# Performance work log

Measured on AMD Instinct MI355X. Metric: run time of the kernel, lower is better.

The kernel has to match this reference:

```python
import jax, jax.numpy as jnp
import numpy as np

N_OUT = 128
N_PARAMS = 64
DEGREE = 3
LB = -3.0
UB = 3.0
N_POINTS = 1048576


def get_knots():
    # (ub-lb) * [zeros(degree), linspace(0,1,n_params-degree), ones(degree)] + lb
    t = np.concatenate([np.zeros(DEGREE), np.linspace(0.0, 1.0, N_PARAMS - DEGREE), np.ones(DEGREE)])
    return jnp.asarray((UB - LB) * t + LB, dtype=jnp.float32)  # [n_params + degree]


def eval_basis(x, knots):
    # x: [N], knots: [n_knots] with n_knots = n_params + degree
    n_knots = knots.shape[0]
    xb = x[:, None]  # [N,1]
    # degree-0 indicator functions, vectorized over all knot intervals
    phis = ((knots[:-1] <= xb) & (xb < knots[1:])).astype(x.dtype)  # [N, n_knots-1]
    # Cox-de Boor recursion, vectorized over basis index i for each degree d
    for d in range(1, DEGREE + 1):
        m = n_knots - d - 1
        ld = knots[d:d + m] - knots[:m]          # left denominators  [m]
        rd = knots[d + 1:d + 1 + m] - knots[1:1 + m]  # right denominators [m]
        left = jnp.where(ld != 0, (xb - knots[:m]) / jnp.where(ld != 0, ld, 1.0), 0.0)
        right = jnp.where(rd != 0, (knots[d + 1:d + 1 + m] - xb) / jnp.where(rd != 0, rd, 1.0), 0.0)
        new = left * phis[:, :m] + right * phis[:, 1:m + 1]
        phis = jnp.concatenate([new, phis[:, m:]], axis=1)
    # last used column is replaced by SiLU(x) (column n_knots - degree - 1 == n_params - 1)
    phis = phis.at[:, n_knots - DEGREE - 1].set(jax.nn.silu(x))
    return phis[:, :N_PARAMS]  # [N, n_params]


def setup_inputs() -> dict:
    key = jax.random.key(0)
    k1, k2 = jax.random.split(key)
    x = jax.random.normal(k1, (N_POINTS,), dtype=jnp.float32)
    params = jax.random.normal(k2, (N_PARAMS, N_OUT), dtype=jnp.float32) * 0.1
    return {"x": x, "params": params}


def reference(x, params):
    knots = get_knots()
    basis = eval_basis(x, knots)          # [N, n_params]
    return (basis @ params).T             # [n_out, N]
```

## Files before the change

kernel.cpp:

```cpp
#include <hip/hip_runtime.h>

#define NPTS 1048576
#define NOUT 128
#define NPAR 64
#define BLOCK 256
#define PPT 4
#define CPB (BLOCK * PPT)
#define STRH 136
#define G 8
#define SST 1024

typedef float vf4 __attribute__((ext_vector_type(4)));

__device__ __forceinline__ unsigned short f2bf(float f) {
    unsigned int u = __float_as_uint(f);
    u += 0x7fffu + ((u >> 16) & 1u);
    return (unsigned short)(u >> 16);
}

__device__ __forceinline__ void bf2x(unsigned int u, float& lo, float& hi) {
    lo = __uint_as_float(u << 16);
    hi = __uint_as_float(u & 0xffff0000u);
}

__global__ __launch_bounds__(BLOCK, 4)
void kan_kernel(const float* __restrict__ x,
                const float* __restrict__ params,
                float* __restrict__ out) {
    __shared__ unsigned short sH[NPAR * STRH];
    __shared__ float sS[G * SST];

    const int tid = threadIdx.x;

    {
        const float4* p4 = (const float4*)params;
        #pragma unroll
        for (int g = tid; g < NPAR * (NOUT / 4); g += BLOCK) {
            float4 v = p4[g];
            ushort4 h;
            h.x = f2bf(v.x); h.y = f2bf(v.y); h.z = f2bf(v.z); h.w = f2bf(v.w);
            *(ushort4*)&sH[(g >> 5) * STRH + (g & 31) * 4] = h;
        }
    }

    const int base = blockIdx.x * CPB + tid * PPT;
    const float4 xv = *(const float4*)(x + base);
    float xs[PPT] = {xv.x, xv.y, xv.z, xv.w};

    float b[PPT][4];
    float sil[PPT];
    int   rbase[PPT];

    #pragma unroll
    for (int pp = 0; pp < PPT; ++pp) {
        float xx = xs[pp];
        sil[pp] = xx / (1.0f + __expf(-xx));

        float inr = (xx >= -3.0f && xx < 3.0f) ? 1.0f : 0.0f;
        float u = (xx + 3.0f) * 10.0f;
        int si = (int)u;
        si = si < 0 ? 0 : (si > 59 ? 59 : si);

        float Ki   = -3.0f + 0.1f * (float)si;
        float Kim1 = -3.0f + 0.1f * (float)(si - 1 > 0 ? si - 1 : 0);
        float Kim2 = -3.0f + 0.1f * (float)(si - 2 > 0 ? si - 2 : 0);
        float Kip1 = -3.0f + 0.1f * (float)(si + 1);
        float Kip2 = -3.0f + 0.1f * (float)(si + 2 < 60 ? si + 2 : 60);
        float Kip3 = -3.0f + 0.1f * (float)(si + 3 < 60 ? si + 3 : 60);

        float l1 = xx - Ki,   r1 = Kip1 - xx;
        float l2 = xx - Kim1, r2 = Kip2 - xx;
        float l3 = xx - Kim2, r3 = Kip3 - xx;

        float N0 = 1.0f, N1, N2, N3, t, saved;
        t = N0 / (r1 + l1); N0 = r1 * t; N1 = l1 * t;
        t = N0 / (r1 + l2); N0 = r1 * t;          saved = l2 * t;
        t = N1 / (r2 + l1); N1 = saved + r2 * t;  N2    = l1 * t;
        t = N0 / (r1 + l3); N0 = r1 * t;          saved = l3 * t;
        t = N1 / (r2 + l2); N1 = saved + r2 * t;  saved = l2 * t;
        t = N2 / (r3 + l1); N2 = saved + r3 * t;  N3    = l1 * t;

        b[pp][0] = N0 * inr;
        b[pp][1] = N1 * inr;
        b[pp][2] = N2 * inr;
        b[pp][3] = N3 * inr;
        rbase[pp] = si;
    }

    __syncthreads();

    const int w = tid >> 6;
    const int l = tid & 63;

    #pragma unroll 1
    for (int j0 = 0; j0 < NOUT; j0 += G) {
        uint4 u63 = *(const uint4*)&sH[63 * STRH + j0];
        float p63f[8];
        bf2x(u63.x, p63f[0], p63f[1]);
        bf2x(u63.y, p63f[2], p63f[3]);
        bf2x(u63.z, p63f[4], p63f[5]);
        bf2x(u63.w, p63f[6], p63f[7]);

        float a[PPT][8];
        #pragma unroll
        for (int pp = 0; pp < PPT; ++pp) {
            const unsigned short* rp = &sH[rbase[pp] * STRH + j0];
            float s = sil[pp];
            float acc[8];
            #pragma unroll
            for (int c = 0; c < 8; ++c) acc[c] = s * p63f[c];

            #pragma unroll
            for (int r = 0; r < 4; ++r) {
                uint4 q = *(const uint4*)(rp + r * STRH);
                float f[8];
                bf2x(q.x, f[0], f[1]); bf2x(q.y, f[2], f[3]);
                bf2x(q.z, f[4], f[5]); bf2x(q.w, f[6], f[7]);
                float br = b[pp][r];
                #pragma unroll
                for (int c = 0; c < 8; ++c) acc[c] = fmaf(br, f[c], acc[c]);
            }
            #pragma unroll
            for (int c = 0; c < 8; ++c) a[pp][c] = acc[c];
        }

        #pragma unroll
        for (int c = 0; c < 8; ++c) {
            vf4 v = { a[0][c], a[1][c], a[2][c], a[3][c] };
            *(vf4*)&sS[c * SST + tid * 4] = v;
        }

        __syncthreads();

        #pragma unroll
        for (int rr = 0; rr < 2; ++rr) {
            const int r = 2 * w + rr;
            float* orow = out + (size_t)(j0 + r) * NPTS + blockIdx.x * CPB;
            #pragma unroll
            for (int k = 0; k < 4; ++k) {
                vf4 v = *(const vf4*)&sS[r * SST + k * 256 + l * 4];
                *(vf4*)(orow + k * 256 + l * 4) = v;
            }
        }

        __syncthreads();
    }
}

extern "C" void kernel_launch(void* const* d_in, const int* in_sizes, int n_in,
                              void* d_out, int out_size, void* d_ws, size_t ws_size,
                              hipStream_t stream) {
    const float* x      = (const float*)d_in[0];
    const float* params = (const float*)d_in[1];
    float* out          = (float*)d_out;

    dim3 grid(NPTS / CPB);
    kan_kernel<<<grid, BLOCK, 0, stream>>>(x, params, out);
}
```

Measured before the change: 120.2 us.

## Warp-specialize producer/consumer waves with double-buffered bf16 LDS ring

Splits each 512-thread block into four compute waves that evaluate the spline basis and matmul tile, and four store waves that stream finished tiles to global memory. Tiles pass through a two-slot LDS ring guarded by workgroup-scope atomic counters instead of block-wide barriers, so compute and stores can overlap. Intermediate tiles are staged as bf16 to halve the LDS footprint, which rounds outputs to bf16 precision. Spin-wait polling and higher register pressure at the larger block size are added costs.

```diff
diff --git a/kernel.cpp b/kernel.cpp
--- a/kernel.cpp
+++ b/kernel.cpp
@@ -3,12 +3,10 @@
 #define NPTS 1048576
 #define NOUT 128
 #define NPAR 64
-#define BLOCK 256
-#define PPT 4
-#define CPB (BLOCK * PPT)
+#define BLOCK 512
+#define CPB 1024
 #define STRH 136
-#define G 8
-#define SST 1024
+#define NTILE 16
 
 typedef float vf4 __attribute__((ext_vector_type(4)));
 
@@ -28,122 +26,148 @@
                 const float* __restrict__ params,
                 float* __restrict__ out) {
     __shared__ unsigned short sH[NPAR * STRH];
-    __shared__ float sS[G * SST];
+    __shared__ unsigned short sRing[2][8 * CPB];
+    __shared__ int prodCnt[2];
+    __shared__ int consCnt[2];
 
     const int tid = threadIdx.x;
+    const int w   = tid >> 6;
+    const int l   = tid & 63;
 
-    {
+    if (tid == 0) { prodCnt[0] = prodCnt[1] = consCnt[0] = consCnt[1] = 0; }
+
+    float b[4][4], sil[4];
+    int rbase[4];
+    if (w < 4) {
         const float4* p4 = (const float4*)params;
         #pragma unroll
-        for (int g = tid; g < NPAR * (NOUT / 4); g += BLOCK) {
+        for (int g = tid; g < NPAR * (NOUT / 4); g += 256) {
             float4 v = p4[g];
             ushort4 h;
             h.x = f2bf(v.x); h.y = f2bf(v.y); h.z = f2bf(v.z); h.w = f2bf(v.w);
             *(ushort4*)&sH[(g >> 5) * STRH + (g & 31) * 4] = h;
         }
-    }
 
-    const int base = blockIdx.x * CPB + tid * PPT;
-    const float4 xv = *(const float4*)(x + base);
-    float xs[PPT] = {xv.x, xv.y, xv.z, xv.w};
+        const int base = blockIdx.x * CPB + tid * 4;
+        const float4 xv = *(const float4*)(x + base);
+        float xs[4] = {xv.x, xv.y, xv.z, xv.w};
 
-    float b[PPT][4];
-    float sil[PPT];
-    int   rbase[PPT];
+        #pragma unroll
+        for (int pp = 0; pp < 4; ++pp) {
+            float xx = xs[pp];
+            sil[pp] = xx / (1.0f + __expf(-xx));
+            float inr = (xx >= -3.0f && xx < 3.0f) ? 1.0f : 0.0f;
+            float u = (xx + 3.0f) * 10.0f;
+            int si = (int)u;
+            si = si < 0 ? 0 : (si > 59 ? 59 : si);
 
-    #pragma unroll
-    for (int pp = 0; pp < PPT; ++pp) {
-        float xx = xs[pp];
-        sil[pp] = xx / (1.0f + __expf(-xx));
+            float Ki   = -3.0f + 0.1f * (float)si;
+            float Kim1 = -3.0f + 0.1f * (float)(si - 1 > 0 ? si - 1 : 0);
+            float Kim2 = -3.0f + 0.1f * (float)(si - 2 > 0 ? si - 2 : 0);
+            float Kip1 = -3.0f + 0.1f * (float)(si + 1);
+            float Kip2 = -3.0f + 0.1f * (float)(si + 2 < 60 ? si + 2 : 60);
+            float Kip3 = -3.0f + 0.1f * (float)(si + 3 < 60 ? si + 3 : 60);
 
-        float inr = (xx >= -3.0f && xx < 3.0f) ? 1.0f : 0.0f;
-        float u = (xx + 3.0f) * 10.0f;
-        int si = (int)u;
-        si = si < 0 ? 0 : (si > 59 ? 59 : si);
+            float l1 = xx - Ki,   r1 = Kip1 - xx;
+            float l2 = xx - Kim1, r2 = Kip2 - xx;
+            float l3 = xx - Kim2, r3 = Kip3 - xx;
 
-        float Ki   = -3.0f + 0.1f * (float)si;
-        float Kim1 = -3.0f + 0.1f * (float)(si - 1 > 0 ? si - 1 : 0);
-        float Kim2 = -3.0f + 0.1f * (float)(si - 2 > 0 ? si - 2 : 0);
-        float Kip1 = -3.0f + 0.1f * (float)(si + 1);
-        float Kip2 = -3.0f + 0.1f * (float)(si + 2 < 60 ? si + 2 : 60);
-        float Kip3 = -3.0f + 0.1f * (float)(si + 3 < 60 ? si + 3 : 60);
+            float N0 = 1.0f, N1, N2, N3, t, saved;
+            t = N0 / (r1 + l1); N0 = r1 * t; N1 = l1 * t;
+            t = N0 / (r1 + l2); N0 = r1 * t;          saved = l2 * t;
+            t = N1 / (r2 + l1); N1 = saved + r2 * t;  N2    = l1 * t;
+            t = N0 / (r1 + l3); N0 = r1 * t;          saved = l3 * t;
+            t = N1 / (r2 + l2); N1 = saved + r2 * t;  saved = l2 * t;
+            t = N2 / (r3 + l1); N2 = saved + r3 * t;  N3    = l1 * t;
 
-        float l1 = xx - Ki,   r1 = Kip1 - xx;
-        float l2 = xx - Kim1, r2 = Kip2 - xx;
-        float l3 = xx - Kim2, r3 = Kip3 - xx;
-
-        float N0 = 1.0f, N1, N2, N3, t, saved;
-        t = N0 / (r1 + l1); N0 = r1 * t; N1 = l1 * t;
-        t = N0 / (r1 + l2); N0 = r1 * t;          saved = l2 * t;
-        t = N1 / (r2 + l1); N1 = saved + r2 * t;  N2    = l1 * t;
-        t = N0 / (r1 + l3); N0 = r1 * t;          saved = l3 * t;
-        t = N1 / (r2 + l2); N1 = saved + r2 * t;  saved = l2 * t;
-        t = N2 / (r3 + l1); N2 = saved + r3 * t;  N3    = l1 * t;
-
-        b[pp][0] = N0 * inr;
-        b[pp][1] = N1 * inr;
-        b[pp][2] = N2 * inr;
-        b[pp][3] = N3 * inr;
-        rbase[pp] = si;
+            b[pp][0] = N0 * inr; b[pp][1] = N1 * inr;
+            b[pp][2] = N2 * inr; b[pp][3] = N3 * inr;
+            rbase[pp] = si;
+        }
     }
 
     __syncthreads();
 
-    const int w = tid >> 6;
-    const int l = tid & 63;
+    if (w < 4) {
+        #pragma unroll 1
+        for (int t = 0; t < NTILE; ++t) {
+            const int s = t & 1, g = t >> 1;
+            if (g > 0) {
+                while (__hip_atomic_load(&consCnt[s], __ATOMIC_ACQUIRE,
+                                         __HIP_MEMORY_SCOPE_WORKGROUP) < 4 * g)
+                    __builtin_amdgcn_s_sleep(1);
+            }
+            const int j0 = t << 3;
 
-    #pragma unroll 1
-    for (int j0 = 0; j0 < NOUT; j0 += G) {
-        uint4 u63 = *(const uint4*)&sH[63 * STRH + j0];
-        float p63f[8];
-        bf2x(u63.x, p63f[0], p63f[1]);
-        bf2x(u63.y, p63f[2], p63f[3]);
-        bf2x(u63.z, p63f[4], p63f[5]);
-        bf2x(u63.w, p63f[6], p63f[7]);
+            uint4 u63 = *(const uint4*)&sH[63 * STRH + j0];
+            float p63f[8];
+            bf2x(u63.x, p63f[0], p63f[1]); bf2x(u63.y, p63f[2], p63f[3]);
+            bf2x(u63.z, p63f[4], p63f[5]); bf2x(u63.w, p63f[6], p63f[7]);
 
-        float a[PPT][8];
-        #pragma unroll
-        for (int pp = 0; pp < PPT; ++pp) {
-            const unsigned short* rp = &sH[rbase[pp] * STRH + j0];
-            float s = sil[pp];
-            float acc[8];
+            float a[4][8];
             #pragma unroll
-            for (int c = 0; c < 8; ++c) acc[c] = s * p63f[c];
+            for (int pp = 0; pp < 4; ++pp) {
+                const unsigned short* rp = &sH[rbase[pp] * STRH + j0];
+                float sv = sil[pp];
+                float acc[8];
+                #pragma unroll
+                for (int c = 0; c < 8; ++c) acc[c] = sv * p63f[c];
+                #pragma unroll
+                for (int r = 0; r < 4; ++r) {
+                    uint4 q = *(const uint4*)(rp + r * STRH);
+                    float f[8];
+                    bf2x(q.x, f[0], f[1]); bf2x(q.y, f[2], f[3]);
+                    bf2x(q.z, f[4], f[5]); bf2x(q.w, f[6], f[7]);
+                    float br = b[pp][r];
+                    #pragma unroll
+                    for (int c = 0; c < 8; ++c) acc[c] = fmaf(br, f[c], acc[c]);
+                }
+                #pragma unroll
+                for (int c = 0; c < 8; ++c) a[pp][c] = acc[c];
+            }
 
             #pragma unroll
-            for (int r = 0; r < 4; ++r) {
-                uint4 q = *(const uint4*)(rp + r * STRH);
-                float f[8];
-                bf2x(q.x, f[0], f[1]); bf2x(q.y, f[2], f[3]);
-                bf2x(q.z, f[4], f[5]); bf2x(q.w, f[6], f[7]);
-                float br = b[pp][r];
+            for (int c = 0; c < 8; ++c) {
+                ushort4 h;
+                h.x = f2bf(a[0][c]); h.y = f2bf(a[1][c]);
+                h.z = f2bf(a[2][c]); h.w = f2bf(a[3][c]);
+                *(ushort4*)&sRing[s][c * CPB + tid * 4] = h;
+            }
+            if (l == 0)
+                __hip_atomic_fetch_add(&prodCnt[s], 1, __ATOMIC_RELEASE,
+                                       __HIP_MEMORY_SCOPE_WORKGROUP);
+        }
+    } else {
+        const int cw = w - 4;
+        float* outb = out + blockIdx.x * CPB;
+        #pragma unroll 1
+        for (int t = 0; t < NTILE; ++t) {
+            const int s = t & 1, g = t >> 1;
+            while (__hip_atomic_load(&prodCnt[s], __ATOMIC_ACQUIRE,
+                                     __HIP_MEMORY_SCOPE_WORKGROUP) < 4 * (g + 1))
+                __builtin_amdgcn_s_sleep(1);
+
+            const int j0 = t << 3;
+            #pragma unroll
+            for (int rr = 0; rr < 2; ++rr) {
+                const int c = 2 * cw + rr;
+                float* orow = outb + (size_t)(j0 + c) * NPTS;
                 #pragma unroll
-                for (int c = 0; c < 8; ++c) acc[c] = fmaf(br, f[c], acc[c]);
+                for (int k = 0; k < 2; ++k) {
+                    uint4 q = *(const uint4*)&sRing[s][c * CPB + k * 512 + l * 8];
+                    float f[8];
+                    bf2x(q.x, f[0], f[1]); bf2x(q.y, f[2], f[3]);
+                    bf2x(q.z, f[4], f[5]); bf2x(q.w, f[6], f[7]);
+                    vf4 v0 = { f[0], f[1], f[2], f[3] };
+                    vf4 v1 = { f[4], f[5], f[6], f[7] };
+                    *(vf4*)(orow + k * 512 + l * 8)     = v0;
+                    *(vf4*)(orow + k * 512 + l * 8 + 4) = v1;
+                }
             }
-            #pragma unroll
-            for (int c = 0; c < 8; ++c) a[pp][c] = acc[c];
+            if (l == 0)
+                __hip_atomic_fetch_add(&consCnt[s], 1, __ATOMIC_RELEASE,
+                                       __HIP_MEMORY_SCOPE_WORKGROUP);
         }
-
-        #pragma unroll
-        for (int c = 0; c < 8; ++c) {
-            vf4 v = { a[0][c], a[1][c], a[2][c], a[3][c] };
-            *(vf4*)&sS[c * SST + tid * 4] = v;
-        }
-
-        __syncthreads();
-
-        #pragma unroll
-        for (int rr = 0; rr < 2; ++rr) {
-            const int r = 2 * w + rr;
-            float* orow = out + (size_t)(j0 + r) * NPTS + blockIdx.x * CPB;
-            #pragma unroll
-            for (int k = 0; k < 4; ++k) {
-                vf4 v = *(const vf4*)&sS[r * SST + k * 256 + l * 4];
-                *(vf4*)(orow + k * 256 + l * 4) = v;
-            }
-        }
-
-        __syncthreads();
     }
 }
 
```

Measured after the change: 140.6 us. 17.0% more time.
